# Optimization experiments

Measured on AMD Instinct MI355X. Metric: run time of the kernel, lower is better.

Reference implementation:

```python
import jax, jax.numpy as jnp
import numpy as np

B, S, D_MODEL, H, D_KV = 2, 2048, 1024, 16, 64
NUM_BUCKETS, MAX_DIST = 32, 128


def _relative_position_bucket(rel_pos, num_buckets=NUM_BUCKETS, max_distance=MAX_DIST):
    # bidirectional (encoder) bucketing, matching T5Attention._relative_position_bucket
    nb = num_buckets // 2
    buckets = (rel_pos > 0).astype(jnp.int32) * nb
    rel = jnp.abs(rel_pos)
    max_exact = nb // 2
    is_small = rel < max_exact
    rel_f = jnp.maximum(rel.astype(jnp.float32), 1.0)  # guard log(0); masked by is_small anyway
    large = max_exact + (
        jnp.log(rel_f / max_exact) / np.log(max_distance / max_exact) * (nb - max_exact)
    ).astype(jnp.int32)
    large = jnp.minimum(large, nb - 1)
    return buckets + jnp.where(is_small, rel, large)


def setup_inputs() -> dict:
    key = jax.random.key(0)
    ks = jax.random.split(key, 6)
    sc = 1.0 / np.sqrt(D_MODEL)
    return {
        "hidden_states": jax.random.normal(ks[0], (B, S, D_MODEL), jnp.float32),
        "Wq": jax.random.normal(ks[1], (D_MODEL, H * D_KV), jnp.float32) * sc,
        "Wk": jax.random.normal(ks[2], (D_MODEL, H * D_KV), jnp.float32) * sc,
        "Wv": jax.random.normal(ks[3], (D_MODEL, H * D_KV), jnp.float32) * sc,
        "Wo": jax.random.normal(ks[4], (H * D_KV, D_MODEL), jnp.float32) * sc,
        "rel_bias_table": jax.random.normal(ks[5], (NUM_BUCKETS, H), jnp.float32),
    }


def reference(hidden_states, Wq, Wk, Wv, Wo, rel_bias_table):
    b, s, _ = hidden_states.shape
    # projections (T5 uses no bias, scale=1.0 in attention)
    q = (hidden_states @ Wq).reshape(b, s, H, D_KV).transpose(0, 2, 1, 3)  # bhsd
    k = (hidden_states @ Wk).reshape(b, s, H, D_KV).transpose(0, 2, 1, 3)
    v = (hidden_states @ Wv).reshape(b, s, H, D_KV).transpose(0, 2, 1, 3)

    # relative position bias: [1, H, S, S]
    ctx = jnp.arange(s)[:, None]
    mem = jnp.arange(s)[None, :]
    buckets = _relative_position_bucket(mem - ctx)          # [S, S]
    pos_bias = rel_bias_table[buckets]                       # [S, S, H]
    pos_bias = pos_bias.transpose(2, 0, 1)[None]             # [1, H, S, S]

    scores = jnp.einsum("bhqd,bhkd->bhqk", q, k) + pos_bias  # scale = 1.0
    probs = jax.nn.softmax(scores, axis=-1)
    attn = jnp.einsum("bhqk,bhkd->bhqd", probs, v)
    attn = attn.transpose(0, 2, 1, 3).reshape(b, s, H * D_KV)
    return attn @ Wo
```

## Files before the change

kernel.cpp:

```cpp
#include <hip/hip_runtime.h>
#include <hip/hip_fp16.h>

#define S_LEN 2048
#define NH 16
#define DK 64
#define DM 1024
#define NB 2
#define QKV_SZ (NB * NH * S_LEN * DK)

typedef _Float16 half8 __attribute__((ext_vector_type(8)));
typedef _Float16 half4v __attribute__((ext_vector_type(4)));
typedef __fp16 fp16x2 __attribute__((ext_vector_type(2)));
typedef float f32x4 __attribute__((ext_vector_type(4)));

static __device__ __forceinline__ half4v pack4(const f32x4 v) {
  fp16x2 lo = __builtin_amdgcn_cvt_pkrtz(v[0], v[1]);
  fp16x2 hi = __builtin_amdgcn_cvt_pkrtz(v[2], v[3]);
  half4v r;
  ((fp16x2*)&r)[0] = lo;
  ((fp16x2*)&r)[1] = hi;
  return r;
}

#define GLL(gp, lp)                                                              \
  __builtin_amdgcn_global_load_lds(                                              \
      (const __attribute__((address_space(1))) unsigned int*)(gp),               \
      (__attribute__((address_space(3))) unsigned int*)(lp), 16, 0, 0)


__global__ __launch_bounds__(256) void conv_f32_f16(const float* __restrict__ in,
                                                    _Float16* __restrict__ out, int n4) {
  int i = blockIdx.x * 256 + threadIdx.x;
  if (i >= n4) return;
  float4 v = ((const float4*)in)[i];
  half4v o;
  o[0] = (_Float16)v.x; o[1] = (_Float16)v.y; o[2] = (_Float16)v.z; o[3] = (_Float16)v.w;
  ((half4v*)out)[i] = o;
}

__global__ __launch_bounds__(256) void transpose_conv4(
    const float* __restrict__ Wq, const float* __restrict__ Wk,
    const float* __restrict__ Wv, const float* __restrict__ Wo,
    _Float16* __restrict__ Wqkvt, _Float16* __restrict__ Wot) {
  __shared__ float tile[32][33];
  int z = blockIdx.z;
  const float* W = (z == 0) ? Wq : (z == 1) ? Wk : (z == 2) ? Wv : Wo;
  _Float16* Wt = (z < 3) ? (Wqkvt + (size_t)z * 1048576) : Wot;
  float scale = (z == 0) ? 1.44269504f : 1.0f;
  int tx = threadIdx.x, ty = threadIdx.y;
  int nx = blockIdx.x * 32 + tx;
  int ky = blockIdx.y * 32;
#pragma unroll
  for (int i = 0; i < 32; i += 8) tile[ty + i][tx] = W[(size_t)(ky + ty + i) * DM + nx];
  __syncthreads();
  int kx = ky + tx;
  int ny = blockIdx.x * 32;
#pragma unroll
  for (int i = 0; i < 32; i += 8)
    Wt[(size_t)(ny + ty + i) * DM + kx] = (_Float16)(tile[tx][ty + i] * scale);
}

__global__ __launch_bounds__(256) void bias_tab_kernel(const float* __restrict__ table,
                                                       float* __restrict__ tab) {
  int i = blockIdx.x * 256 + threadIdx.x;
  if (i >= NH * 4095) return;
  int h = i / 4095, r = i - h * 4095;
  int rel = r - 2047;
  int bucket = rel > 0 ? 16 : 0;
  int a = rel < 0 ? -rel : rel;
  if (a < 8) {
    bucket += a;
  } else {
    int lg = 31 - __clz(a * a);
    int large = 8 + (lg - 6);
    bucket += (large < 15 ? large : 15);
  }
  tab[i] = table[bucket * NH + h] * 1.44269504f;
}

template <int MODE>
__global__ __launch_bounds__(256) void gemm_f16(const _Float16* __restrict__ A,
                                                const _Float16* __restrict__ Bt,
                                                void* __restrict__ Cout,
                                                int M, int N, int K) {
  __shared__ _Float16 As[128 * 32];
  __shared__ _Float16 Bs[128 * 32];
  const int t = threadIdx.x;
  const int gx = gridDim.x;
  const int nwg = gx * gridDim.y;
  const int orig = blockIdx.x + gx * blockIdx.y;
  const int wg = (orig & 7) * (nwg >> 3) + (orig >> 3);
  const int m0 = (wg / gx) * 128, n0 = (wg % gx) * 128;
  const int w = t >> 6, lane = t & 63, l15 = lane & 15, quad = lane >> 4;
  const int wr = (w >> 1) * 64, wc = (w & 1) * 64;
  const int swz = (quad ^ (l15 & 3)) * 8;

  f32x4 acc[4][4];
#pragma unroll
  for (int i = 0; i < 4; i++)
#pragma unroll
    for (int j = 0; j < 4; j++) acc[i][j] = (f32x4){0.f, 0.f, 0.f, 0.f};

  for (int k0 = 0; k0 < K; k0 += 32) {
    __syncthreads();
#pragma unroll
    for (int i = 0; i < 2; i++) {
      int id = t + 256 * i;
      int row = id >> 2, c = id & 3;
      int cg = c ^ (row & 3);
      GLL(A + (size_t)(m0 + row) * K + k0 + cg * 8, (char*)As + id * 16);
      GLL(Bt + (size_t)(n0 + row) * K + k0 + cg * 8, (char*)Bs + id * 16);
    }
    __syncthreads();
    half8 af[4], bf[4];
#pragma unroll
    for (int i = 0; i < 4; i++) af[i] = *(const half8*)(As + (wr + i * 16 + l15) * 32 + swz);
#pragma unroll
    for (int i = 0; i < 4; i++) bf[i] = *(const half8*)(Bs + (wc + i * 16 + l15) * 32 + swz);
#pragma unroll
    for (int i = 0; i < 4; i++)
#pragma unroll
      for (int j = 0; j < 4; j++)
        acc[i][j] = __builtin_amdgcn_mfma_f32_16x16x32_f16(af[i], bf[j], acc[i][j], 0, 0, 0);
  }

#pragma unroll
  for (int i = 0; i < 4; i++)
#pragma unroll
    for (int j = 0; j < 4; j++) {
      int row0 = m0 + wr + i * 16 + quad * 4;
      int col = n0 + wc + j * 16 + l15;
      if (MODE == 1) {
#pragma unroll
        for (int r = 0; r < 4; r++)
          ((float*)Cout)[(size_t)(row0 + r) * N + col] = acc[i][j][r];
      } else {
        int which = col >> 10, rem = col & 1023, hh = rem >> 6, dd = rem & 63;
        int bb = row0 >> 11, ss = row0 & 2047;
        _Float16* base = (_Float16*)Cout;
        if (which == 2) {
          *(half4v*)(base + (size_t)2 * QKV_SZ +
                     ((size_t)((bb * NH + hh) * DK + dd)) * S_LEN + ss) = pack4(acc[i][j]);
        } else {
#pragma unroll
          for (int r = 0; r < 4; r++)
            base[(size_t)which * QKV_SZ +
                 ((size_t)((bb * NH + hh) * S_LEN) + ss + r) * DK + dd] = (_Float16)acc[i][j][r];
        }
      }
    }
}

__global__ __launch_bounds__(256) void gemm_f16_n64(const _Float16* __restrict__ A,
                                                    const _Float16* __restrict__ Bt,
                                                    float* __restrict__ C,
                                                    int M, int N, int K) {
  __shared__ _Float16 As[128 * 32];
  __shared__ _Float16 Bs[64 * 32];
  const int t = threadIdx.x;
  const int gx = gridDim.x;
  const int nwg = gx * gridDim.y;
  const int orig = blockIdx.x + gx * blockIdx.y;
  const int wg = (orig & 7) * (nwg >> 3) + (orig >> 3);
  const int m0 = (wg / gx) * 128, n0 = (wg % gx) * 64;
  const int w = t >> 6, lane = t & 63, l15 = lane & 15, quad = lane >> 4;
  const int wr = (w >> 1) * 64, wc = (w & 1) * 32;
  const int swz = (quad ^ (l15 & 3)) * 8;

  f32x4 acc[4][2];
#pragma unroll
  for (int i = 0; i < 4; i++)
#pragma unroll
    for (int j = 0; j < 2; j++) acc[i][j] = (f32x4){0.f, 0.f, 0.f, 0.f};

  for (int k0 = 0; k0 < K; k0 += 32) {
    __syncthreads();
#pragma unroll
    for (int i = 0; i < 2; i++) {
      int id = t + 256 * i;
      int row = id >> 2, c = id & 3;
      int cg = c ^ (row & 3);
      GLL(A + (size_t)(m0 + row) * K + k0 + cg * 8, (char*)As + id * 16);
    }
    {
      int row = t >> 2, c = t & 3;
      int cg = c ^ (row & 3);
      GLL(Bt + (size_t)(n0 + row) * K + k0 + cg * 8, (char*)Bs + t * 16);
    }
    __syncthreads();
    half8 af[4], bf[2];
#pragma unroll
    for (int i = 0; i < 4; i++) af[i] = *(const half8*)(As + (wr + i * 16 + l15) * 32 + swz);
#pragma unroll
    for (int j = 0; j < 2; j++) bf[j] = *(const half8*)(Bs + (wc + j * 16 + l15) * 32 + swz);
#pragma unroll
    for (int i = 0; i < 4; i++)
#pragma unroll
      for (int j = 0; j < 2; j++)
        acc[i][j] = __builtin_amdgcn_mfma_f32_16x16x32_f16(af[i], bf[j], acc[i][j], 0, 0, 0);
  }

#pragma unroll
  for (int i = 0; i < 4; i++)
#pragma unroll
    for (int j = 0; j < 2; j++) {
      int row0 = m0 + wr + i * 16 + quad * 4;
      int col = n0 + wc + j * 16 + l15;
#pragma unroll
      for (int r = 0; r < 4; r++)
        C[(size_t)(row0 + r) * N + col] = acc[i][j][r];
    }
}

__global__ __launch_bounds__(256, 4) void attn_kernel(
    const _Float16* __restrict__ Q, const _Float16* __restrict__ K,
    const _Float16* __restrict__ Vt, const float* __restrict__ btab,
    _Float16* __restrict__ attn_out) {
  __shared__ _Float16 Ks[2][4096];
  __shared__ _Float16 Vs[2][4096];
  __shared__ float slab[512];

  const int t = threadIdx.x;
  const int orig = blockIdx.x + (blockIdx.y << 5) + (blockIdx.z << 9);
  const int wg = (orig & 7) * 128 + (orig >> 3);
  const int Q0 = (wg & 31) * 64;
  const int h = (wg >> 5) & 15, b = wg >> 9;
  const int w = t >> 6, lane = t & 63, l15 = lane & 15, quad = lane >> 4;
  const int qw0 = Q0 + w * 16;
  const int sw7 = l15 & 7;

  const _Float16* Qb = Q + (size_t)(b * NH + h) * S_LEN * DK;
  const _Float16* Kb = K + (size_t)(b * NH + h) * S_LEN * DK;
  const _Float16* Vb = Vt + (size_t)(b * NH + h) * S_LEN * DK;

  for (int i = t; i < 512; i += 256) slab[i] = btab[h * 4095 + 1791 + i];
  const float cbn = btab[h * 4095 + 1791 + 128];
  const float cbp = btab[h * 4095 + 1791 + 384];

  const int id0 = t, id1 = t + 256;
  const int r0_ = id0 >> 3, cg0 = (id0 & 7) ^ (r0_ & 7), p0 = r0_ & 31;
  const int sr0 = (r0_ & 32) | (((p0 >> 2) & 3) << 3) | ((p0 >> 4) << 2) | (p0 & 3);
  const int r1_ = id1 >> 3, cg1 = (id1 & 7) ^ (r1_ & 7), p1 = r1_ & 31;
  const int sr1 = (r1_ & 32) | (((p1 >> 2) & 3) << 3) | ((p1 >> 4) << 2) | (p1 & 3);
  const int kofa = sr0 * DK + cg0 * 8, kofb = sr1 * DK + cg1 * 8;
  const int vofa = r0_ * S_LEN + cg0 * 8, vofb = r1_ * S_LEN + cg1 * 8;
  const int lda = id0 * 16, ldb = id1 * 16;

#define STAGE(bs, kk0)                                   \
  do {                                                   \
    const _Float16* kp_ = Kb + (size_t)(kk0) * DK;       \
    const _Float16* vp_ = Vb + (kk0);                    \
    GLL(kp_ + kofa, (char*)Ks[bs] + lda);                \
    GLL(kp_ + kofb, (char*)Ks[bs] + ldb);                \
    GLL(vp_ + vofa, (char*)Vs[bs] + lda);                \
    GLL(vp_ + vofb, (char*)Vs[bs] + ldb);                \
  } while (0)

  half8 qf[2];
#pragma unroll
  for (int dh = 0; dh < 2; dh++)
    qf[dh] = *(const half8*)(Qb + (size_t)(qw0 + l15) * DK + dh * 32 + quad * 8);

  f32x4 o[4];
#pragma unroll
  for (int dt = 0; dt < 4; dt++) o[dt] = (f32x4){0.f, 0.f, 0.f, 0.f};
  f32x4 lac = (f32x4){0.f, 0.f, 0.f, 0.f};
  float m_ = -INFINITY;
  const half4v ones = {(_Float16)1.f, (_Float16)1.f, (_Float16)1.f, (_Float16)1.f};

  const int rd0 = l15 * 64 + (quad ^ sw7) * 8;
  const int rd1 = rd0 ^ 32;

  STAGE(0, 0);
  __syncthreads();

#define TILE(c, kk, stage_ok)                                                         \
  do {                                                                                \
    if (stage_ok) STAGE((c) ^ 1, (kk) + 64);   \
    const int dk0 = (kk) - qw0;                                                       \
    const bool farneg = (dk0 <= -191);                                                \
    const bool farpos = (dk0 >= 143);                                                 \
    const bool nearc = !(farneg || farpos);                                           \
    const float cb = farneg ? cbn : cbp;                                              \
    f32x4 st[4];                                                                      \
    if (nearc) {                                                                      \
      _Pragma("unroll") for (int kt = 0; kt < 4; kt++) {                              \
        int i0 = dk0 + (kt >> 1) * 32 + quad * 8 + (kt & 1) * 4 - l15 + 256;          \
        f32x4 v_;                                                                     \
        v_[0] = slab[i0]; v_[1] = slab[i0 + 1];                                       \
        v_[2] = slab[i0 + 2]; v_[3] = slab[i0 + 3];                                   \
        st[kt] = v_;                                                                  \
      }                                                                               \
    } else {                                                                          \
      _Pragma("unroll") for (int kt = 0; kt < 4; kt++)                                \
          st[kt] = (f32x4){0.f, 0.f, 0.f, 0.f};                                       \
    }                                                                                 \
    half8 kf0[4], kf1[4];                                                             \
    _Pragma("unroll") for (int kt = 0; kt < 4; kt++) {                                \
      kf0[kt] = *(const half8*)(&Ks[c][rd0 + kt * 1024]);                             \
      kf1[kt] = *(const half8*)(&Ks[c][rd1 + kt * 1024]);                             \
    }                                                                                 \
    __builtin_amdgcn_s_setprio(1);                                                    \
    _Pragma("unroll") for (int kt = 0; kt < 4; kt++) {                                \
      st[kt] = __builtin_amdgcn_mfma_f32_16x16x32_f16(kf0[kt], qf[0], st[kt], 0, 0, 0); \
      st[kt] = __builtin_amdgcn_mfma_f32_16x16x32_f16(kf1[kt], qf[1], st[kt], 0, 0, 0); \
    }                                                                                 \
    __builtin_amdgcn_s_setprio(0);                                                    \
                                                         \
    float x0 = fmaxf(fmaxf(st[0][0], st[0][1]), st[0][2]);                            \
    float x1 = fmaxf(fmaxf(st[0][3], st[1][0]), st[1][1]);                            \
    float x2 = fmaxf(fmaxf(st[1][2], st[1][3]), st[2][0]);                            \
    float x3 = fmaxf(fmaxf(st[2][1], st[2][2]), st[2][3]);                            \
    float x4 = fmaxf(fmaxf(st[3][0], st[3][1]), st[3][2]);                            \
    float cm = fmaxf(fmaxf(fmaxf(x0, x1), fmaxf(x2, x3)), fmaxf(x4, st[3][3]));       \
    cm = fmaxf(cm, __shfl_xor(cm, 16));                                               \
    cm = fmaxf(cm, __shfl_xor(cm, 32));                                               \
    float mc = nearc ? cm : cm + cb;                                                  \
    if (__any(mc > m_ + 8.f)) {     \
      float mnew = fmaxf(m_, mc);                                                     \
      float alpha = __builtin_amdgcn_exp2f(m_ - mnew);                                \
      m_ = mnew;                                                                      \
      lac *= alpha;                                                                   \
      _Pragma("unroll") for (int dt = 0; dt < 4; dt++) o[dt] *= alpha;                \
    }                                                                                 \
    float msub = nearc ? m_ : m_ - cb;                                                \
    half4v p16[4];                                                                    \
    _Pragma("unroll") for (int kt = 0; kt < 4; kt++) {                                \
      f32x4 p_;                                                                       \
      _Pragma("unroll") for (int r = 0; r < 4; r++)                                   \
          p_[r] = __builtin_amdgcn_exp2f(st[kt][r] - msub);                           \
      p16[kt] = pack4(p_);                                                            \
    }                                                                                 \
    __builtin_amdgcn_s_setprio(1);                                                    \
     \
    _Pragma("unroll") for (int kt = 0; kt < 4; kt++)                                  \
        lac = __builtin_amdgcn_mfma_f32_16x16x16f16(ones, p16[kt], lac, 0, 0, 0);     \
    _Pragma("unroll") for (int dt = 0; dt < 4; dt++) {                                \
      half8 va_ = *(const half8*)(&Vs[c][rd0 + dt * 1024]);                           \
      half8 vb_ = *(const half8*)(&Vs[c][rd1 + dt * 1024]);                           \
      half4v alo = {va_[0], va_[1], va_[2], va_[3]};                                  \
      half4v ahi = {va_[4], va_[5], va_[6], va_[7]};                                  \
      half4v blo = {vb_[0], vb_[1], vb_[2], vb_[3]};                                  \
      half4v bhi = {vb_[4], vb_[5], vb_[6], vb_[7]};                                  \
      o[dt] = __builtin_amdgcn_mfma_f32_16x16x16f16(alo, p16[0], o[dt], 0, 0, 0);     \
      o[dt] = __builtin_amdgcn_mfma_f32_16x16x16f16(ahi, p16[1], o[dt], 0, 0, 0);     \
      o[dt] = __builtin_amdgcn_mfma_f32_16x16x16f16(blo, p16[2], o[dt], 0, 0, 0);     \
      o[dt] = __builtin_amdgcn_mfma_f32_16x16x16f16(bhi, p16[3], o[dt], 0, 0, 0);     \
    }                                                                                 \
    __builtin_amdgcn_s_setprio(0);                                                    \
    __syncthreads();              \
  } while (0)

  for (int k0 = 0; k0 < S_LEN; k0 += 128) {
    TILE(0, k0, 1);
    TILE(1, k0 + 64, (k0 + 128 < S_LEN));
  }
#undef TILE
#undef STAGE

  float inv = 1.0f / lac[0];
  int q = qw0 + l15;
#pragma unroll
  for (int dt = 0; dt < 4; dt++) {
    f32x4 ov = o[dt] * inv;
    *(half4v*)(attn_out + ((size_t)(b * S_LEN + q)) * DM + h * DK + dt * 16 + quad * 4) =
        pack4(ov);
  }
}

extern "C" void kernel_launch(void* const* d_in, const int* in_sizes, int n_in,
                              void* d_out, int out_size, void* d_ws, size_t ws_size,
                              hipStream_t stream) {
  const float* hs  = (const float*)d_in[0];
  const float* Wq  = (const float*)d_in[1];
  const float* Wk  = (const float*)d_in[2];
  const float* Wv  = (const float*)d_in[3];
  const float* Wo  = (const float*)d_in[4];
  const float* tbl = (const float*)d_in[5];
  float* out = (float*)d_out;
  char* ws = (char*)d_ws;

  _Float16* Xh    = (_Float16*)(ws);
  _Float16* Wqkvt = (_Float16*)(ws + (8u << 20));
  _Float16* Wot   = (_Float16*)(ws + (14u << 20));
  _Float16* Qd    = (_Float16*)(ws + (16u << 20));
  _Float16* Kd    = Qd + (size_t)QKV_SZ;
  _Float16* Vd    = Qd + (size_t)2 * QKV_SZ;
  _Float16* Ah    = (_Float16*)(ws + (40u << 20));
  float*    btab  = (float*)(ws + (48u << 20));

  conv_f32_f16<<<4096, 256, 0, stream>>>(hs, Xh, (NB * S_LEN * DM) / 4);
  transpose_conv4<<<dim3(32, 32, 4), dim3(32, 8), 0, stream>>>(Wq, Wk, Wv, Wo, Wqkvt, Wot);
  bias_tab_kernel<<<256, 256, 0, stream>>>(tbl, btab);

  gemm_f16<0><<<dim3(24, 32), 256, 0, stream>>>(Xh, Wqkvt, (void*)Qd, NB * S_LEN, 3 * DM, DM);
  attn_kernel<<<dim3(S_LEN / 64, NH, NB), 256, 0, stream>>>(Qd, Kd, Vd, btab, Ah);
  gemm_f16_n64<<<dim3(16, 32), 256, 0, stream>>>(Ah, Wot, out, NB * S_LEN, DM, DM);
}
```

Measured before the change: 208.3 us.

## Double-buffer LDS tiles in projection GEMMs to overlap loads with MFMA

Both GEMM kernels now use two LDS buffers per operand. The next k-tile is prefetched through direct global-to-LDS loads while MFMAs run on the current tile, which replaces two barriers per iteration with one. Load address offsets are precomputed outside the loop and the loop is unrolled by two. This doubles LDS use per block and could lower occupancy. It assumes K is a multiple of 64.

Result: faster. 202.2 us (-2.9%).

```diff
diff --git a/kernel.cpp b/kernel.cpp
--- a/kernel.cpp
+++ b/kernel.cpp
@@ -83,8 +83,8 @@
                                                 const _Float16* __restrict__ Bt,
                                                 void* __restrict__ Cout,
                                                 int M, int N, int K) {
-  __shared__ _Float16 As[128 * 32];
-  __shared__ _Float16 Bs[128 * 32];
+  __shared__ _Float16 As[2][128 * 32];
+  __shared__ _Float16 Bs[2][128 * 32];
   const int t = threadIdx.x;
   const int gx = gridDim.x;
   const int nwg = gx * gridDim.y;
@@ -95,34 +95,51 @@
   const int wr = (w >> 1) * 64, wc = (w & 1) * 64;
   const int swz = (quad ^ (l15 & 3)) * 8;
 
+  const int row0_ = t >> 2, cg0 = (t & 3) ^ (row0_ & 3);
+  const int row1_ = (t + 256) >> 2, cg1 = ((t + 256) & 3) ^ (row1_ & 3);
+  const int aof0 = row0_ * K + cg0 * 8, aof1 = row1_ * K + cg1 * 8;
+  const int lda = t * 16, ldb = (t + 256) * 16;
+
   f32x4 acc[4][4];
 #pragma unroll
   for (int i = 0; i < 4; i++)
 #pragma unroll
     for (int j = 0; j < 4; j++) acc[i][j] = (f32x4){0.f, 0.f, 0.f, 0.f};
 
-  for (int k0 = 0; k0 < K; k0 += 32) {
-    __syncthreads();
-#pragma unroll
-    for (int i = 0; i < 2; i++) {
-      int id = t + 256 * i;
-      int row = id >> 2, c = id & 3;
-      int cg = c ^ (row & 3);
-      GLL(A + (size_t)(m0 + row) * K + k0 + cg * 8, (char*)As + id * 16);
-      GLL(Bt + (size_t)(n0 + row) * K + k0 + cg * 8, (char*)Bs + id * 16);
-    }
-    __syncthreads();
-    half8 af[4], bf[4];
-#pragma unroll
-    for (int i = 0; i < 4; i++) af[i] = *(const half8*)(As + (wr + i * 16 + l15) * 32 + swz);
-#pragma unroll
-    for (int i = 0; i < 4; i++) bf[i] = *(const half8*)(Bs + (wc + i * 16 + l15) * 32 + swz);
-#pragma unroll
-    for (int i = 0; i < 4; i++)
-#pragma unroll
-      for (int j = 0; j < 4; j++)
-        acc[i][j] = __builtin_amdgcn_mfma_f32_16x16x32_f16(af[i], bf[j], acc[i][j], 0, 0, 0);
+#define GSTAGE(bs, kk)                                                     \
+  do {                                                                     \
+    const _Float16* ap_ = A + (size_t)m0 * K + (kk);                       \
+    const _Float16* bp_ = Bt + (size_t)n0 * K + (kk);                      \
+    GLL(ap_ + aof0, (char*)As[bs] + lda);                                  \
+    GLL(ap_ + aof1, (char*)As[bs] + ldb);                                  \
+    GLL(bp_ + aof0, (char*)Bs[bs] + lda);                                  \
+    GLL(bp_ + aof1, (char*)Bs[bs] + ldb);                                  \
+  } while (0)
+
+  GSTAGE(0, 0);
+  __syncthreads();
+
+#define GTILE(c, kk)                                                          \
+  do {                                                                        \
+    if ((kk) + 32 < K) GSTAGE((c) ^ 1, (kk) + 32);                            \
+    half8 af[4], bf[4];                                                       \
+    _Pragma("unroll") for (int i = 0; i < 4; i++)                             \
+        af[i] = *(const half8*)(As[c] + (wr + i * 16 + l15) * 32 + swz);      \
+    _Pragma("unroll") for (int i = 0; i < 4; i++)                             \
+        bf[i] = *(const half8*)(Bs[c] + (wc + i * 16 + l15) * 32 + swz);      \
+    _Pragma("unroll") for (int i = 0; i < 4; i++)                             \
+        _Pragma("unroll") for (int j = 0; j < 4; j++)                         \
+            acc[i][j] =                                                       \
+                __builtin_amdgcn_mfma_f32_16x16x32_f16(af[i], bf[j], acc[i][j], 0, 0, 0); \
+    __syncthreads();                                                          \
+  } while (0)
+
+  for (int k0 = 0; k0 < K; k0 += 64) {
+    GTILE(0, k0);
+    GTILE(1, k0 + 32);
   }
+#undef GTILE
+#undef GSTAGE
 
 #pragma unroll
   for (int i = 0; i < 4; i++)
@@ -155,8 +172,8 @@
                                                     const _Float16* __restrict__ Bt,
                                                     float* __restrict__ C,
                                                     int M, int N, int K) {
-  __shared__ _Float16 As[128 * 32];
-  __shared__ _Float16 Bs[64 * 32];
+  __shared__ _Float16 As[2][128 * 32];
+  __shared__ _Float16 Bs[2][64 * 32];
   const int t = threadIdx.x;
   const int gx = gridDim.x;
   const int nwg = gx * gridDim.y;
@@ -167,38 +184,50 @@
   const int wr = (w >> 1) * 64, wc = (w & 1) * 32;
   const int swz = (quad ^ (l15 & 3)) * 8;
 
+  const int row0_ = t >> 2, cg0 = (t & 3) ^ (row0_ & 3);
+  const int row1_ = (t + 256) >> 2, cg1 = ((t + 256) & 3) ^ (row1_ & 3);
+  const int aof0 = row0_ * K + cg0 * 8, aof1 = row1_ * K + cg1 * 8;
+  const int lda = t * 16, ldb = (t + 256) * 16;
+
   f32x4 acc[4][2];
 #pragma unroll
   for (int i = 0; i < 4; i++)
 #pragma unroll
     for (int j = 0; j < 2; j++) acc[i][j] = (f32x4){0.f, 0.f, 0.f, 0.f};
 
-  for (int k0 = 0; k0 < K; k0 += 32) {
-    __syncthreads();
-#pragma unroll
-    for (int i = 0; i < 2; i++) {
-      int id = t + 256 * i;
-      int row = id >> 2, c = id & 3;
-      int cg = c ^ (row & 3);
-      GLL(A + (size_t)(m0 + row) * K + k0 + cg * 8, (char*)As + id * 16);
-    }
-    {
-      int row = t >> 2, c = t & 3;
-      int cg = c ^ (row & 3);
-      GLL(Bt + (size_t)(n0 + row) * K + k0 + cg * 8, (char*)Bs + t * 16);
-    }
-    __syncthreads();
-    half8 af[4], bf[2];
-#pragma unroll
-    for (int i = 0; i < 4; i++) af[i] = *(const half8*)(As + (wr + i * 16 + l15) * 32 + swz);
-#pragma unroll
-    for (int j = 0; j < 2; j++) bf[j] = *(const half8*)(Bs + (wc + j * 16 + l15) * 32 + swz);
-#pragma unroll
-    for (int i = 0; i < 4; i++)
-#pragma unroll
-      for (int j = 0; j < 2; j++)
-        acc[i][j] = __builtin_amdgcn_mfma_f32_16x16x32_f16(af[i], bf[j], acc[i][j], 0, 0, 0);
+#define GSTAGE(bs, kk)                                                     \
+  do {                                                                     \
+    const _Float16* ap_ = A + (size_t)m0 * K + (kk);                       \
+    const _Float16* bp_ = Bt + (size_t)n0 * K + (kk);                      \
+    GLL(ap_ + aof0, (char*)As[bs] + lda);                                  \
+    GLL(ap_ + aof1, (char*)As[bs] + ldb);                                  \
+    GLL(bp_ + aof0, (char*)Bs[bs] + lda);                                  \
+  } while (0)
+
+  GSTAGE(0, 0);
+  __syncthreads();
+
+#define GTILE(c, kk)                                                          \
+  do {                                                                        \
+    if ((kk) + 32 < K) GSTAGE((c) ^ 1, (kk) + 32);                            \
+    half8 af[4], bf[2];                                                       \
+    _Pragma("unroll") for (int i = 0; i < 4; i++)                             \
+        af[i] = *(const half8*)(As[c] + (wr + i * 16 + l15) * 32 + swz);      \
+    _Pragma("unroll") for (int j = 0; j < 2; j++)                             \
+        bf[j] = *(const half8*)(Bs[c] + (wc + j * 16 + l15) * 32 + swz);      \
+    _Pragma("unroll") for (int i = 0; i < 4; i++)                             \
+        _Pragma("unroll") for (int j = 0; j < 2; j++)                         \
+            acc[i][j] =                                                       \
+                __builtin_amdgcn_mfma_f32_16x16x32_f16(af[i], bf[j], acc[i][j], 0, 0, 0); \
+    __syncthreads();                                                          \
+  } while (0)
+
+  for (int k0 = 0; k0 < K; k0 += 64) {
+    GTILE(0, k0);
+    GTILE(1, k0 + 32);
   }
+#undef GTILE
+#undef GSTAGE
 
 #pragma unroll
   for (int i = 0; i < 4; i++)
```
